# Optimization experiments

Measured on AMD Instinct MI355X. Metric: run time of the kernel, lower is better.

The kernel has to match this reference:

```python
import jax, jax.numpy as jnp
import numpy as np

EPS = 1e-5
B, C, H, W, MIP, CQ = 2, 256, 64, 64, 8, 32  # MIP = max(8, C//32); CQ = C//8


def _bn(x, p):
    # inference BatchNorm; p is [4, C] = (gamma, beta, running_mean, running_var)
    g, b, m, v = p[0], p[1], p[2], p[3]
    s = g / jnp.sqrt(v + EPS)
    return x * s[None, :, None, None] + (b - m * s)[None, :, None, None]


def _c1(x, w):  # 1x1 conv, w: [O, I]
    return jnp.einsum('bchw,oc->bohw', x, w)


def _c3(x, w):  # 3x3 conv, SAME padding, w: [O, I, 3, 3]
    return jax.lax.conv_general_dilated(x, w, (1, 1), 'SAME',
                                        dimension_numbers=('NCHW', 'OIHW', 'NCHW'))


def _cbs1(x, w, p):  # Conv(1x1)+BN+SiLU (YOLOv7 Conv block)
    return jax.nn.silu(_bn(_c1(x, w), p))


def _cbs3(x, w, p):  # Conv(3x3)+BN+SiLU
    return jax.nn.silu(_bn(_c3(x, w), p))


def _maxpool(x, k):  # MaxPool2d(kernel=k, stride=1, padding=k//2)
    p = k // 2
    return jax.lax.reduce_window(x, -jnp.inf, jax.lax.max,
                                 (1, 1, k, k), (1, 1, 1, 1),
                                 ((0, 0), (0, 0), (p, p), (p, p)))


def setup_inputs() -> dict:
    ks = iter(jax.random.split(jax.random.key(0), 64))

    def rn(shape, scale):
        return jax.random.normal(next(ks), shape, jnp.float32) * scale

    def w_(o, i, k=1):  # fan-in scaled conv weight
        sc = 1.0 / float(np.sqrt(i * k * k))
        return rn((o, i) if k == 1 else (o, i, k, k), sc)

    def bnp(c):  # gamma, beta, running_mean, running_var (var > 0)
        return jnp.stack([1.0 + rn((c,), 0.05), rn((c,), 0.05), rn((c,), 0.05),
                          0.5 + jax.random.uniform(next(ks), (c,), jnp.float32)])

    cm = C  # SPPCSPC hidden: int(2*C*0.5) = C
    return dict(
        x=rn((B, C, H, W), 1.0),
        ca_w1=w_(MIP, C), ca_b1=rn((MIP,), 0.05), ca_bn=bnp(MIP),
        ca_wh=w_(C, MIP), ca_bh=rn((C,), 0.05),
        ca_ww=w_(C, MIP), ca_bw=rn((C,), 0.05),
        s1_w=w_(cm, C), s1_bn=bnp(cm),
        s2_w=w_(cm, C), s2_bn=bnp(cm),
        s3_w=w_(cm, cm, 3), s3_bn=bnp(cm),
        s4_w=w_(cm, cm), s4_bn=bnp(cm),
        s5_w=w_(cm, 4 * cm), s5_bn=bnp(cm),
        s6_w=w_(cm, cm, 3), s6_bn=bnp(cm),
        s7_w=w_(C, 2 * cm), s7_bn=bnp(C),
        pq_w=w_(CQ, C), pq_b=rn((CQ,), 0.05),
        pk_w=w_(CQ, C), pk_b=rn((CQ,), 0.05),
        pv_w=w_(C, C), pv_b=rn((C,), 0.05),
        gamma_pa=rn((1,), 1.0), gamma_ca=rn((1,), 1.0),
    )


def reference(x, ca_w1, ca_b1, ca_bn, ca_wh, ca_bh, ca_ww, ca_bw,
              s1_w, s1_bn, s2_w, s2_bn, s3_w, s3_bn, s4_w, s4_bn,
              s5_w, s5_bn, s6_w, s6_bn, s7_w, s7_bn,
              pq_w, pq_b, pk_w, pk_b, pv_w, pv_b, gamma_pa, gamma_ca):
    b, c, h, w = x.shape
    # ---- CoordAtt ----
    xh = jnp.mean(x, axis=3, keepdims=True)                                 # b,c,h,1
    xw = jnp.transpose(jnp.mean(x, axis=2, keepdims=True), (0, 1, 3, 2))    # b,c,w,1
    y = jnp.concatenate([xh, xw], axis=2)                                   # b,c,h+w,1
    y = _bn(_c1(y, ca_w1) + ca_b1[None, :, None, None], ca_bn)
    y = y * jnp.clip(y + 3.0, 0.0, 6.0) / 6.0                               # h_swish
    a_h = jax.nn.sigmoid(_c1(y[:, :, :h], ca_wh) + ca_bh[None, :, None, None])
    a_w = jax.nn.sigmoid(_c1(jnp.transpose(y[:, :, h:], (0, 1, 3, 2)), ca_ww)
                         + ca_bw[None, :, None, None])
    r = x * a_w * a_h
    # ---- SPPCSPC ----
    x1 = _cbs1(_cbs3(_cbs1(r, s1_w, s1_bn), s3_w, s3_bn), s4_w, s4_bn)
    cat = jnp.concatenate([x1] + [_maxpool(x1, k) for k in (5, 9, 13)], axis=1)
    y1 = _cbs3(_cbs1(cat, s5_w, s5_bn), s6_w, s6_bn)
    y2 = _cbs1(r, s2_w, s2_bn)
    res = _cbs1(jnp.concatenate([y1, y2], axis=1), s7_w, s7_bn)
    # ---- PAM (spatial attention) ----
    n = h * w
    f = res.reshape(b, c, n)
    q = jnp.einsum('bcn,oc->bon', f, pq_w) + pq_b[None, :, None]            # b,c/8,n
    k = jnp.einsum('bcn,oc->bon', f, pk_w) + pk_b[None, :, None]
    v = jnp.einsum('bcn,oc->bon', f, pv_w) + pv_b[None, :, None]            # b,c,n
    attn = jax.nn.softmax(jnp.einsum('bcn,bcm->bnm', q, k), axis=-1)        # b,n,n
    res_pa = gamma_pa * jnp.einsum('bcm,bnm->bcn', v, attn).reshape(b, c, h, w) + res
    # ---- CAM (channel attention) ----
    e = jnp.einsum('bcn,bdn->bcd', f, f)                                    # b,c,c
    attn_c = jax.nn.softmax(jnp.max(e, axis=-1, keepdims=True) - e, axis=-1)
    res_ca = gamma_ca * jnp.einsum('bcd,bdn->bcn', attn_c, f).reshape(b, c, h, w) + res
    return res + res_ca + res_pa
```

## Files before the change

### kernel.cpp

```cpp
#include <hip/hip_runtime.h>

typedef unsigned short u16;
typedef __attribute__((ext_vector_type(8))) short bf16x8;
typedef __attribute__((ext_vector_type(4))) float f32x4;
#define EPSV 1e-5f
#define LOG2E 1.4426950408889634f

__device__ __forceinline__ float b2f(u16 u) {
  union { float f; unsigned int i; } v; v.i = ((unsigned int)u) << 16; return v.f;
}
__device__ __forceinline__ u16 f2b(float f) {
  union { float f; unsigned int i; } v; v.f = f;
  unsigned int r = v.i + 0x7FFFu + ((v.i >> 16) & 1u);
  return (u16)(r >> 16);
}
__device__ __forceinline__ u16 f2b_trunc(float f) {
  union { float f; unsigned int i; } v; v.f = f;
  return (u16)(v.i >> 16);
}
__device__ __forceinline__ float silu_(float z) { return z / (1.f + exp2f(-LOG2E * z)); }

__global__ __launch_bounds__(128) void detect_k(const u16* __restrict__ xp, float* __restrict__ flag) {
  __shared__ int cnt[2];
  int t = threadIdx.x;
// ... 55 lines not shown
  union { u16 h[8]; uint4 q; } u;
  u.h[0]=f2b(f0.x); u.h[1]=f2b(f0.y); u.h[2]=f2b(f0.z); u.h[3]=f2b(f0.w);
  u.h[4]=f2b(f1.x); u.h[5]=f2b(f1.y); u.h[6]=f2b(f1.z); u.h[7]=f2b(f1.w);
  *(uint4*)(dst + (long)i * 8) = u.q;
}


__global__ __launch_bounds__(256) void plane_means(const float* __restrict__ x, float* __restrict__ yin) {
  __shared__ float pl[4096];
  int bc = blockIdx.x, t = threadIdx.x;
  const float* xp = x + (long)bc * 4096;
  for (int j = 0; j < 16; ++j) { int id = j * 256 + t; pl[id] = xp[id]; }
  __syncthreads();
  if (t < 64) {
    float s = 0.f;
    for (int w = 0; w < 64; ++w) s += pl[t * 64 + w];
    yin[(long)bc * 128 + t] = s * (1.f / 64.f);
  } else if (t < 128) {
    int w = t - 64; float s = 0.f;
    for (int h = 0; h < 64; ++h) s += pl[h * 64 + w];
    yin[(long)bc * 128 + 64 + w] = s * (1.f / 64.f);
  }
}

__global__ __launch_bounds__(128) void ca_conv1(const float* __restrict__ yin, const float* __restrict__ w1,
                                                const float* __restrict__ b1, const float* __restrict__ bnp,
                                                float* __restrict__ ybn) {
  int b = blockIdx.x, p = threadIdx.x;
  float acc[8] = {0.f,0.f,0.f,0.f,0.f,0.f,0.f,0.f};
  for (int c = 0; c < 256; ++c) {
    float yv = yin[((long)b * 256 + c) * 128 + p];
    #pragma unroll
    for (int o = 0; o < 8; ++o) acc[o] += w1[o * 256 + c] * yv;
  }
  #pragma unroll
  for (int o = 0; o < 8; ++o) {
    float z = acc[o] + b1[o];
    float g = bnp[o], bt = bnp[8 + o], mn = bnp[16 + o], vr = bnp[24 + o];
    float s = g * rsqrtf(vr + EPSV);
    z = z * s + (bt - mn * s);
    float hs = fminf(fmaxf(z + 3.f, 0.f), 6.f) * (1.f / 6.f);
    ybn[((long)b * 8 + o) * 128 + p] = z * hs;
  }
}

__global__ __launch_bounds__(128) void ca_gate(const float* __restrict__ ybn,
    const float* __restrict__ wh, const float* __restrict__ bh,
    const float* __restrict__ ww, const float* __restrict__ bw,
    float* __restrict__ ah, float* __restrict__ aw_) {
  int c = blockIdx.x, b = blockIdx.y, t = threadIdx.x;
  if (t < 64) {
    float d = 0.f;
    #pragma unroll
    for (int o = 0; o < 8; ++o) d += wh[c * 8 + o] * ybn[((long)b * 8 + o) * 128 + t];
    d += bh[c];
    ah[((long)b * 256 + c) * 64 + t] = 1.f / (1.f + exp2f(-LOG2E * d));
  } else {
    int w = t - 64;
    float d = 0.f;
    #pragma unroll
    for (int o = 0; o < 8; ++o) d += ww[c * 8 + o] * ybn[((long)b * 8 + o) * 128 + 64 + w];
    d += bw[c];
    aw_[((long)b * 256 + c) * 64 + w] = 1.f / (1.f + exp2f(-LOG2E * d));
  }
}

__global__ __launch_bounds__(256) void apply_ca(const float* __restrict__ x, const float* __restrict__ ah,
                                                const float* __restrict__ aw_, u16* __restrict__ r) {
  int idx = blockIdx.x * 256 + threadIdx.x;
  int n = idx & 4095, bc = idx >> 12;
  int h = n >> 6, w = n & 63;
  r[idx] = f2b(x[idx] * ah[bc * 64 + h] * aw_[bc * 64 + w]);
}


template<int ACT, int OUTH>
__global__ __launch_bounds__(256) void mfma_cbs(
    const u16* __restrict__ Wbf, long aBS,
    const u16* __restrict__ In, long bBS,
    void* __restrict__ Out, long oBS,
    int O, int K, int N,
    const float* __restrict__ bnp, const float* __restrict__ bias)
{
  __shared__ u16 Bs[64 * 40];
  __shared__ float albe[64][2];
  const int t = threadIdx.x;
  const int n0 = blockIdx.x * 64;
  const int o0 = blockIdx.y * 64;
  const int b  = blockIdx.z;
  const int w = t >> 6, l = t & 63, lq = l >> 4, lr = l & 15;
  const int wo = (w >> 1) * 32, wn = (w & 1) * 32;
  if (t < 64) {
    int o = o0 + t;
    float al = 1.f, be = 0.f;
    if (bnp) {
      float g = bnp[o], bt = bnp[O + o], mn = bnp[2 * O + o], vr = bnp[3 * O + o];
      al = g * rsqrtf(vr + EPSV); be = bt - mn * al;
    }
    if (bias) be += bias[o];
    albe[t][0] = al; albe[t][1] = be;
  }
  const u16* Ab = Wbf + (long)b * aBS;
  const u16* inb = In + (long)b * bBS + n0;
  const u16* a0p = Ab + (long)(o0 + wo + lr) * K + lq * 8;
  const u16* a1p = a0p + (long)16 * K;
  const int bk = t >> 3, bn8 = (t & 7) * 8;
  f32x4 acc[2][2] = {};
  uint4 a0 = *(const uint4*)(a0p);
  uint4 a1 = *(const uint4*)(a1p);
  uint4 b0 = *(const uint4*)(inb + (long)bk * N + bn8);
  for (int kc = 0; kc < K; kc += 32) {
    int kn = kc + 32; if (kn >= K) kn = 0;
    __syncthreads();
    {
      union { uint4 q; u16 h[8]; } tb; tb.q = b0;
      #pragma unroll
      for (int j = 0; j < 8; ++j) Bs[(bn8 + j) * 40 + bk] = tb.h[j];
    }
    uint4 a0n = *(const uint4*)(a0p + kn);
    uint4 a1n = *(const uint4*)(a1p + kn);
    uint4 b0n = *(const uint4*)(inb + (long)(kn + bk) * N + bn8);
    __syncthreads();
    bf16x8 bfv0 = *(const bf16x8*)&Bs[(wn + lr) * 40 + lq * 8];
    bf16x8 bfv1 = *(const bf16x8*)&Bs[(wn + 16 + lr) * 40 + lq * 8];
    acc[0][0] = __builtin_amdgcn_mfma_f32_16x16x32_bf16(*(const bf16x8*)&a0, bfv0, acc[0][0], 0, 0, 0);
    acc[0][1] = __builtin_amdgcn_mfma_f32_16x16x32_bf16(*(const bf16x8*)&a0, bfv1, acc[0][1], 0, 0, 0);
    acc[1][0] = __builtin_amdgcn_mfma_f32_16x16x32_bf16(*(const bf16x8*)&a1, bfv0, acc[1][0], 0, 0, 0);
    acc[1][1] = __builtin_amdgcn_mfma_f32_16x16x32_bf16(*(const bf16x8*)&a1, bfv1, acc[1][1], 0, 0, 0);
    a0 = a0n; a1 = a1n; b0 = b0n;
  }
  float* ob = (float*)Out + (long)b * oBS;
  u16* obh = (u16*)Out + (long)b * oBS;
  #pragma unroll
  for (int i = 0; i < 2; ++i) {
    #pragma unroll
    for (int r = 0; r < 4; ++r) {
      int ol = wo + i * 16 + lq * 4 + r;
      float al = albe[ol][0], be = albe[ol][1];
      #pragma unroll
      for (int j = 0; j < 2; ++j) {
        float vv = acc[i][j][r] * al + be;
        if (ACT) vv = silu_(vv);
        if (OUTH == 2) {
          int col = n0 + wn + j * 16 + lr;
          obh[((long)(col >> 5) * 256 + (o0 + ol)) * 32 + (col & 31)] = f2b(vv);
        } else if (OUTH) {
          obh[(long)(o0 + ol) * N + n0 + wn + j * 16 + lr] = f2b(vv);
        } else {
          ob[(long)(o0 + ol) * N + n0 + wn + j * 16 + lr] = vv;
        }
      }
    }
  }
}

__global__ __launch_bounds__(256) void conv3_mfma(
    const u16* __restrict__ Wt,
    const u16* __restrict__ In, long iBS,
    u16* __restrict__ Out, long oBS, int O, int I,
    const float* __restrict__ bnp)
{
  __shared__ u16 Bs[4 * 66 * 34];
  __shared__ float albe[64][2];
  const int t = threadIdx.x;
  const int h0 = blockIdx.x * 2;
  const int o0 = blockIdx.y * 64;
  const int b  = blockIdx.z;
  const int w = t >> 6, l = t & 63, lq = l >> 4, lr = l & 15;
  const int wn = w * 32;
  if (t < 64) {
    int o = o0 + t;
    float g = bnp[o], bt = bnp[O + o], mn = bnp[2 * O + o], vr = bnp[3 * O + o];
    float al = g * rsqrtf(vr + EPSV);
    albe[t][0] = al; albe[t][1] = bt - mn * al;
  }
  {
    int r = t >> 6, cs = (t >> 5) & 1, ch = t & 31;
    Bs[(r * 66 + (cs ? 65 : 0)) * 34 + ch] = 0;
  }
  const u16* inb = In + (long)b * iBS;
  const int bch = t >> 3, bcg = (t & 7) * 8;
  const u16* wlane = Wt + (long)(o0 + lr) * 32 + lq * 8;
  const int nC8 = I >> 5;
  f32x4 acc[4][2] = {};

  uint4 tb0, tb1, tb2, tb3;
  {
    const u16* cb = inb + (long)bch * 4096 + bcg;
    tb0 = (h0 - 1 >= 0) ? *(const uint4*)(cb + (h0 - 1) * 64) : make_uint4(0,0,0,0);
    tb1 = *(const uint4*)(cb + h0 * 64);
    tb2 = *(const uint4*)(cb + (h0 + 1) * 64);
    tb3 = (h0 + 2 < 64) ? *(const uint4*)(cb + (h0 + 2) * 64) : make_uint4(0,0,0,0);
  }

  for (int c8 = 0; c8 < nC8; ++c8) {
    __syncthreads();
    {
      union { uint4 q; u16 h[8]; } u0, u1, u2, u3;
      u0.q = tb0; u1.q = tb1; u2.q = tb2; u3.q = tb3;
      #pragma unroll
      for (int j2 = 0; j2 < 8; ++j2) {
        Bs[(0 * 66 + bcg + 1 + j2) * 34 + bch] = u0.h[j2];
        Bs[(1 * 66 + bcg + 1 + j2) * 34 + bch] = u1.h[j2];
        Bs[(2 * 66 + bcg + 1 + j2) * 34 + bch] = u2.h[j2];
        Bs[(3 * 66 + bcg + 1 + j2) * 34 + bch] = u3.h[j2];
      }
    }
    int c8n = c8 + 1; if (c8n >= nC8) c8n = 0;
    uint4 n0_, n1_, n2_, n3_;
    {
      const u16* cb = inb + (long)(c8n * 32 + bch) * 4096 + bcg;
      n0_ = (h0 - 1 >= 0) ? *(const uint4*)(cb + (h0 - 1) * 64) : make_uint4(0,0,0,0);
      n1_ = *(const uint4*)(cb + h0 * 64);
      n2_ = *(const uint4*)(cb + (h0 + 1) * 64);
      n3_ = (h0 + 2 < 64) ? *(const uint4*)(cb + (h0 + 2) * 64) : make_uint4(0,0,0,0);
    }
    __syncthreads();
    const u16* wc8 = wlane + (long)c8 * 9 * 256 * 32;
    #pragma unroll
    for (int dy = 0; dy < 3; ++dy) {
      #pragma unroll
      for (int dx = 0; dx < 3; ++dx) {
        const int tap = dy * 3 + dx;
        const u16* wl = wc8 + (long)tap * 256 * 32;
        uint4 af0 = *(const uint4*)(wl);
        uint4 af1 = *(const uint4*)(wl + 16 * 32);
        uint4 af2 = *(const uint4*)(wl + 32 * 32);
        uint4 af3 = *(const uint4*)(wl + 48 * 32);
        #pragma unroll
        for (int j = 0; j < 2; ++j) {
          int nb = wn + j * 16;
          int rowS = (nb >> 6) + dy;
          int colS = (nb & 63) + dx;
          bf16x8 bv = *(const bf16x8*)&Bs[(rowS * 66 + colS + lr) * 34 + lq * 8];
          acc[0][j] = __builtin_amdgcn_mfma_f32_16x16x32_bf16(*(const bf16x8*)&af0, bv, acc[0][j], 0, 0, 0);
          acc[1][j] = __builtin_amdgcn_mfma_f32_16x16x32_bf16(*(const bf16x8*)&af1, bv, acc[1][j], 0, 0, 0);
          acc[2][j] = __builtin_amdgcn_mfma_f32_16x16x32_bf16(*(const bf16x8*)&af2, bv, acc[2][j], 0, 0, 0);
          acc[3][j] = __builtin_amdgcn_mfma_f32_16x16x32_bf16(*(const bf16x8*)&af3, bv, acc[3][j], 0, 0, 0);
        }
      }
    }
    tb0 = n0_; tb1 = n1_; tb2 = n2_; tb3 = n3_;
  }
  u16* ob = Out + (long)b * oBS;
  const int n0 = h0 * 64;
  #pragma unroll
  for (int i = 0; i < 4; ++i) {
    #pragma unroll
    for (int r = 0; r < 4; ++r) {
      int ol = i * 16 + lq * 4 + r;
      float al = albe[ol][0], be = albe[ol][1];
      #pragma unroll
      for (int j = 0; j < 2; ++j) {
        float vv = silu_(acc[i][j][r] * al + be);
        ob[(long)(o0 + ol) * 4096 + n0 + wn + j * 16 + lr] = f2b(vv);
      }
    }
  }
}

__global__ __launch_bounds__(256) void pool3(u16* __restrict__ cat, long bs) {
  __shared__ float A[68][72];
  __shared__ float Bb[68][72];
  const int t = threadIdx.x;
  const int c = blockIdx.x, b = blockIdx.y;
  u16* base = cat + (long)b * bs + (long)c * 4096;
  for (int i = t; i < 68 * 72; i += 256) { (&A[0][0])[i] = -1e30f; (&Bb[0][0])[i] = -1e30f; }
  __syncthreads();
  const int r = t >> 2, c0 = (t & 3) * 16;
  #pragma unroll
  for (int j = 0; j < 16; ++j) A[r + 2][c0 + 2 + j] = b2f(base[r * 64 + c0 + j]);
  const long CNu = 1048576;
  #pragma unroll 1
  for (int s = 1; s <= 3; ++s) {
    __syncthreads();
    #pragma unroll
    for (int j = 0; j < 16; ++j) {
      int cc = c0 + j;
      float m = fmaxf(fmaxf(fmaxf(A[r+2][cc], A[r+2][cc+1]), fmaxf(A[r+2][cc+2], A[r+2][cc+3])), A[r+2][cc+4]);
      Bb[r + 2][cc + 2] = m;
    }
    __syncthreads();
    u16* out = base + (long)s * CNu;
    #pragma unroll
    for (int j = 0; j < 16; ++j) {
      int hc = c0 + 2 + j;
      float m = fmaxf(fmaxf(fmaxf(Bb[r][hc], Bb[r+1][hc]), fmaxf(Bb[r+2][hc], Bb[r+3][hc])), Bb[r+4][hc]);
      out[r * 64 + c0 + j] = f2b_trunc(m);
      A[r + 2][hc] = m;
    }
  }
}

__global__ __launch_bounds__(256) void transpose_hh(const u16* __restrict__ in, u16* __restrict__ out) {
  __shared__ u16 tile[32][34];
  int b = blockIdx.z;
  int c0 = blockIdx.x * 32, r0 = blockIdx.y * 32;
  int tx = threadIdx.x & 31, ty = threadIdx.x >> 5;
  const u16* ib = in + (long)b * 262144;
  u16* ob = out + (long)b * 262144;
  #pragma unroll
  for (int i = 0; i < 4; ++i) {
    int r = r0 + ty + i * 8;
    tile[ty + i * 8][tx] = ib[(long)r * 4096 + c0 + tx];
  }
  __syncthreads();
  #pragma unroll
  for (int i = 0; i < 4; ++i) {
    int c = c0 + ty + i * 8;
    ob[(long)c * 64 + r0 + tx] = tile[tx][ty + i * 8];
  }
}

__global__ __launch_bounds__(256) void pam_qk_max(const u16* __restrict__ qkT, float* __restrict__ pmax) {
  __shared__ u16 Qs[32 * 40];
  __shared__ u16 Ks[64 * 40];
  __shared__ float red[4][32][17];
  const int t = threadIdx.x;
  const int b = blockIdx.z, ms = blockIdx.y, n0 = blockIdx.x * 32;
  const int w = t >> 6, l = t & 63, lq = l >> 4, lr = l & 15;
  const int wn = w & 1, wc = w >> 1;
  if (t < 128) {
    int row = t >> 2, cq = (t & 3) * 8;
    *(uint4*)&Qs[row * 40 + cq] = *(const uint4*)(qkT + ((long)b * 4096 + n0 + row) * 64 + cq);
  }
  __syncthreads();
  bf16x8 qf = *(const bf16x8*)&Qs[(wn * 16 + lr) * 40 + lq * 8];
  float mx4[4] = {-1e30f, -1e30f, -1e30f, -1e30f};
  const int krow = t >> 2, kcq = (t & 3) * 8;
  for (int it = 0; it < 16; ++it) {
    int m0 = ms * 1024 + it * 64;
    __syncthreads();
    *(uint4*)&Ks[krow * 40 + kcq] = *(const uint4*)(qkT + ((long)b * 4096 + m0 + krow) * 64 + 32 + kcq);
    __syncthreads();
    #pragma unroll
    for (int s = 0; s < 2; ++s) {
      int msub = wc * 2 + s;
      bf16x8 kf = *(const bf16x8*)&Ks[(msub * 16 + lr) * 40 + lq * 8];
      f32x4 S = {};
      S = __builtin_amdgcn_mfma_f32_16x16x32_bf16(qf, kf, S, 0, 0, 0);
      #pragma unroll
      for (int r = 0; r < 4; ++r) mx4[r] = fmaxf(mx4[r], S[r]);
    }
  }
  #pragma unroll
  for (int r = 0; r < 4; ++r) red[w][wn * 16 + lq * 4 + r][lr] = mx4[r];
  __syncthreads();
  if (t < 32) {
    int wbase = t >> 4;
    float M = -1e30f;
    #pragma unroll
    for (int j = 0; j < 2; ++j)
      #pragma unroll
      for (int l2 = 0; l2 < 16; ++l2)
        M = fmaxf(M, red[wbase + 2 * j][t][l2]);
    pmax[((long)ms * 2 + b) * 4096 + n0 + t] = M;
  }
}

__global__ __launch_bounds__(256) void pam_merge(const float* __restrict__ pmax, float* __restrict__ rmx) {
  int i = blockIdx.x * 256 + threadIdx.x;
  int b = i >> 12, n = i & 4095;
  float m = pmax[(long)b * 4096 + n];
  #pragma unroll
  for (int ms = 1; ms < 4; ++ms) m = fmaxf(m, pmax[((long)ms * 2 + b) * 4096 + n]);
  rmx[i] = m;
}

__global__ __launch_bounds__(512) void pam_attn(const u16* __restrict__ qkT,
    const u16* __restrict__ vb, const float* __restrict__ rowmax,
    float* __restrict__ Obase, float* __restrict__ Sbase) {
  __shared__ u16 Qs[32 * 40];
  __shared__ u16 Ks[2][64 * 40];
  __shared__ u16 Ps[32 * 72];
  __shared__ float rmL[32];
  __shared__ float srow[32];
  const int t = threadIdx.x;
  const int mh = blockIdx.y;
  const int b = blockIdx.z;
  const int n0 = blockIdx.x * 32;
  const int w = t >> 6, l = t & 63, lq = l >> 4, lr = l & 15;
  const int nf = w & 1;
  const int mf = w >> 1;
  const int cw = w * 32;
  float* O = Obase + (long)mh * 2097152;
  float* S = Sbase + (long)mh * 8192;
  if (t < 128) {
    int row = t >> 2, cq = (t & 3) * 8;
    *(uint4*)&Qs[row * 40 + cq] = *(const uint4*)(qkT + ((long)b * 4096 + n0 + row) * 64 + cq);
  }
  if (t < 32) { rmL[t] = rowmax[(long)b * 4096 + n0 + t] * LOG2E; srow[t] = 0.f; }
  const int krow = t >> 3, kc4 = (t & 7) * 4;
  const u16* kbase = qkT + ((long)b * 4096 + krow) * 64 + 32 + kc4;
  const u16* vop = vb + (long)b * 1048576 + (cw + lr) * 32 + lq * 8;
  const int mStart = mh * 2048, mEnd = mStart + 2048;

  {
    uint2 k0 = *(const uint2*)(kbase + (long)mStart * 64);
    *(uint2*)&Ks[0][krow * 40 + kc4] = k0;
  }
  uint2 kreg = *(const uint2*)(kbase + (long)(mStart + 64) * 64);
  long vt0 = (long)(mStart >> 5) * 8192;
  uint4 vA00 = *(const uint4*)(vop + vt0);
  uint4 vA01 = *(const uint4*)(vop + vt0 + 512);
  uint4 vA10 = *(const uint4*)(vop + vt0 + 8192);
  uint4 vA11 = *(const uint4*)(vop + vt0 + 8704);
  uint4 vB00, vB01, vB10, vB11;

  __syncthreads();
  bf16x8 qf = *(const bf16x8*)&Qs[(nf * 16 + lr) * 40 + lq * 8];
  const float rml = rmL[nf * 16 + lr];
  float spl = 0.f;
  f32x4 acc[2][2] = {};

#define QK_PHASE(BUF)                                                          \
  {                                                                            \
    bf16x8 kf = *(const bf16x8*)&Ks[BUF][(mf * 16 + lr) * 40 + lq * 8];        \
    f32x4 Sv = {};                                                             \
    Sv = __builtin_amdgcn_mfma_f32_16x16x32_bf16(kf, qf, Sv, 0, 0, 0);         \
    union { u16 h[4]; uint2 q; } pk;                                           \
    _Pragma("unroll")                                                          \
    for (int r = 0; r < 4; ++r) {                                              \
      float p = exp2f(Sv[r] * LOG2E - rml);                                    \
      spl += p;                                                                \
      pk.h[r] = f2b_trunc(p);                                                  \
    }                                                                          \
    *(uint2*)&Ps[(nf * 16 + lr) * 72 + mf * 16 + lq * 4] = pk.q;               \
  }

#define PV_PHASE(V00, V01, V10, V11)                                           \
  {                                                                            \
    bf16x8 pf0 = *(const bf16x8*)&Ps[lr * 72 + lq * 8];                        \
    bf16x8 pf1 = *(const bf16x8*)&Ps[(16 + lr) * 72 + lq * 8];                 \
    acc[0][0] = __builtin_amdgcn_mfma_f32_16x16x32_bf16(*(bf16x8*)&V00, pf0, acc[0][0], 0, 0, 0); \
    acc[0][1] = __builtin_amdgcn_mfma_f32_16x16x32_bf16(*(bf16x8*)&V00, pf1, acc[0][1], 0, 0, 0); \
    acc[1][0] = __builtin_amdgcn_mfma_f32_16x16x32_bf16(*(bf16x8*)&V01, pf0, acc[1][0], 0, 0, 0); \
    acc[1][1] = __builtin_amdgcn_mfma_f32_16x16x32_bf16(*(bf16x8*)&V01, pf1, acc[1][1], 0, 0, 0); \
    pf0 = *(const bf16x8*)&Ps[lr * 72 + 32 + lq * 8];                          \
    pf1 = *(const bf16x8*)&Ps[(16 + lr) * 72 + 32 + lq * 8];                   \
    acc[0][0] = __builtin_amdgcn_mfma_f32_16x16x32_bf16(*(bf16x8*)&V10, pf0, acc[0][0], 0, 0, 0); \
    acc[0][1] = __builtin_amdgcn_mfma_f32_16x16x32_bf16(*(bf16x8*)&V10, pf1, acc[0][1], 0, 0, 0); \
    acc[1][0] = __builtin_amdgcn_mfma_f32_16x16x32_bf16(*(bf16x8*)&V11, pf0, acc[1][0], 0, 0, 0); \
    acc[1][1] = __builtin_amdgcn_mfma_f32_16x16x32_bf16(*(bf16x8*)&V11, pf1, acc[1][1], 0, 0, 0); \
  }

  #pragma unroll 1
  for (int m0 = mStart; m0 < mEnd; m0 += 128) {
    int m2 = m0 + 128; if (m2 >= mEnd) m2 = mStart;
    int m3 = m0 + 192; if (m3 >= mEnd) m3 = mStart;
    QK_PHASE(0)
    *(uint2*)&Ks[1][krow * 40 + kc4] = kreg;
    kreg = *(const uint2*)(kbase + (long)m2 * 64);
    {
      long vt = (long)((m0 + 64) >> 5) * 8192;
      vB00 = *(const uint4*)(vop + vt);
      vB01 = *(const uint4*)(vop + vt + 512);
      vB10 = *(const uint4*)(vop + vt + 8192);
      vB11 = *(const uint4*)(vop + vt + 8704);
    }
    __syncthreads();
    __builtin_amdgcn_s_setprio(1);
    PV_PHASE(vA00, vA01, vA10, vA11)
    __builtin_amdgcn_s_setprio(0);
    __syncthreads();
    QK_PHASE(1)
    *(uint2*)&Ks[0][krow * 40 + kc4] = kreg;
    kreg = *(const uint2*)(kbase + (long)m3 * 64);
    {
      long vt = (long)(m2 >> 5) * 8192;
      vA00 = *(const uint4*)(vop + vt);
      vA01 = *(const uint4*)(vop + vt + 512);
      vA10 = *(const uint4*)(vop + vt + 8192);
      vA11 = *(const uint4*)(vop + vt + 8704);
    }
    __syncthreads();
    __builtin_amdgcn_s_setprio(1);
    PV_PHASE(vB00, vB01, vB10, vB11)
    __builtin_amdgcn_s_setprio(0);
    __syncthreads();
  }
#undef QK_PHASE
#undef PV_PHASE

  spl += __shfl_xor(spl, 16);
  spl += __shfl_xor(spl, 32);
  if (l < 16) atomicAdd(&srow[nf * 16 + lr], spl);
  __syncthreads();
  if (t < 32) S[(long)b * 4096 + n0 + t] = srow[t];
  float* ob = O + (long)b * 1048576 + n0;
  #pragma unroll
  for (int cf = 0; cf < 2; ++cf) {
    #pragma unroll
    for (int r = 0; r < 4; ++r) {
      int c = cw + cf * 16 + lq * 4 + r;
      ob[(long)c * 4096 + lr]      = acc[cf][0][r];
      ob[(long)c * 4096 + 16 + lr] = acc[cf][1][r];
    }
  }
}


__global__ __launch_bounds__(256) void fillz(float* __restrict__ p, int n) {
  int i = blockIdx.x * 256 + threadIdx.x;
  if (i < n) p[i] = 0.f;
}

__global__ __launch_bounds__(256) void cam_e_mfma(const u16* __restrict__ resb, float* __restrict__ e) {
  __shared__ u16 Bs[128 * 40];
  const int t = threadIdx.x;
  const int d0 = blockIdx.x * 128;
  const int c0 = blockIdx.y * 64;
  const int bz = blockIdx.z;
  const int b = bz >> 4, ks = bz & 15;
  const int w = t >> 6, l = t & 63, lq = l >> 4, lr = l & 15;
  const int wo = (w >> 1) * 32, wn = (w & 1) * 64;
  const u16* fb = resb + (long)b * 1048576;
  const u16* a0p = fb + (long)(c0 + wo + lr) * 4096 + lq * 8;
  const u16* a1p = a0p + (long)16 * 4096;
  const int bo = t >> 1, bkq = (t & 1) * 16;
  const u16* bp = fb + (long)(d0 + bo) * 4096 + bkq;
  const int kS = ks * 256, kE = kS + 256;
  f32x4 acc[2][4] = {};
  uint4 a0 = *(const uint4*)(a0p + kS);
  uint4 a1 = *(const uint4*)(a1p + kS);
  uint4 b0 = *(const uint4*)(bp + kS);
  uint4 b1 = *(const uint4*)(bp + kS + 8);
  for (int kc = kS; kc < kE; kc += 32) {
    int kn = kc + 32; if (kn >= kE) kn = kS;
    __syncthreads();
    *(uint4*)&Bs[bo * 40 + bkq] = b0;
    *(uint4*)&Bs[bo * 40 + bkq + 8] = b1;
    uint4 a0n = *(const uint4*)(a0p + kn);
    uint4 a1n = *(const uint4*)(a1p + kn);
    uint4 b0n = *(const uint4*)(bp + kn);
    uint4 b1n = *(const uint4*)(bp + kn + 8);
    __syncthreads();
    #pragma unroll
    for (int j = 0; j < 4; ++j) {
      bf16x8 bfv = *(const bf16x8*)&Bs[(wn + j * 16 + lr) * 40 + lq * 8];
      acc[0][j] = __builtin_amdgcn_mfma_f32_16x16x32_bf16(*(const bf16x8*)&a0, bfv, acc[0][j], 0, 0, 0);
      acc[1][j] = __builtin_amdgcn_mfma_f32_16x16x32_bf16(*(const bf16x8*)&a1, bfv, acc[1][j], 0, 0, 0);
    }
    a0 = a0n; a1 = a1n; b0 = b0n; b1 = b1n;
  }
  #pragma unroll
  for (int i = 0; i < 2; ++i)
    #pragma unroll
    for (int r = 0; r < 4; ++r) {
      int ol = wo + i * 16 + lq * 4 + r;
      #pragma unroll
      for (int j = 0; j < 4; ++j)
        atomicAdd(&e[((long)b << 16) + (long)(c0 + ol) * 256 + d0 + wn + j * 16 + lr], acc[i][j][r]);
    }
}

__global__ __launch_bounds__(256) void cam_softmax(const float* __restrict__ e, u16* __restrict__ attn) {
  __shared__ float red[256];
  int c = blockIdx.x, b = blockIdx.y, t = threadIdx.x;
  const float* row = e + ((long)b << 16) + (long)c * 256;
  float v = row[t];
  red[t] = v; __syncthreads();
  for (int s = 128; s > 0; s >>= 1) { if (t < s) red[t] = fminf(red[t], red[t + s]); __syncthreads(); }
  float emin = red[0]; __syncthreads();
  float ex = exp2f(LOG2E * (emin - v));
  red[t] = ex; __syncthreads();
  for (int s = 128; s > 0; s >>= 1) { if (t < s) red[t] += red[t + s]; __syncthreads(); }
  float inv = 1.f / red[0];
  attn[((long)b << 16) + (long)c * 256 + t] = f2b(ex * inv);
}


__global__ __launch_bounds__(256) void combine(const float* __restrict__ res, const float* __restrict__ O,
    const float* __restrict__ S, const float* __restrict__ cam, const float* __restrict__ gp,
    void* __restrict__ outp, const float* __restrict__ flagp) {
  int idx = blockIdx.x * 256 + threadIdx.x;
  int b = idx >> 20, n = idx & 4095;
  float g1 = gp[0], g2 = gp[1];
  float sden = S[(long)b * 4096 + n] + S[8192 + (long)b * 4096 + n];
  float pamv = (O[idx] + O[2097152 + idx]) / sden;
  float v = 3.f * res[idx] + g1 * pamv + g2 * cam[idx];
  if (*flagp > 0.5f) ((float*)outp)[idx] = v;
  else               ((u16*)outp)[idx] = f2b(v);
}


extern "C" void kernel_launch(void* const* d_in, const int* in_sizes, int n_in,
                              void* d_out, int out_size, void* d_ws, size_t ws_size,
                              hipStream_t stream)
{
  (void)out_size; (void)ws_size; (void)n_in;
  float* ws = (float*)d_ws;
  const long CN = 1048576;

  float* A  = ws;
  float* Bp = ws + 2 * CN;
  float* Cp = ws + 4 * CN;
  float* D  = ws + 6 * CN;
  const long WFo = 14 * CN;

  u16*   rB   = (u16*)A;
  float* res  = A;
  float* xf   = Bp;
  u16*   BpU  = (u16*)Bp;
  float* yin  = Cp;
  float* ybn  = Cp + 65536;
  float* ah   = Cp + 67584;
  float* aw_  = Cp + 100352;
  u16*   CpU  = (u16*)Cp;
  u16*   catU = (u16*)D;
  u16*   y12U = (u16*)D;
  float* D2   = D + 2 * CN;
  u16*   qkbU = (u16*)D2;
  u16*   qkTU = (u16*)(D2 + 262144);
  float* pmax = D2 + 524288;
  float* rmx  = D2 + 557056;
  float* e    = D2 + 565248;
  u16*   attnc= (u16*)(D2 + 696320);
  float* S0   = D2 + 761856;
  float* cam  = D;
  float* O0   = D + 4 * CN;

  ConvArgs ca;
  long fOff[30], hOff[30];
  long hcur = 0;
  float* flagp = ws + WFo;
  {
    long cum = 0, fcur = WFo + 4;
    for (int i = 0; i < 30; ++i) {
      ca.src[i] = d_in[i];
      int h = (i == 8 || i == 10 || i == 14 || i == 16 || i == 20 ||
               i == 22 || i == 24 || i == 26) ? 1 : 0;
      ca.mode[i] = h;
      if (i == 0) { ca.dst[i] = 2 * CN; fOff[i] = 2 * CN; }
      else if (h) { ca.dst[i] = hcur; hOff[i] = hcur; hcur += in_sizes[i]; }
      else        { ca.dst[i] = fcur; fOff[i] = fcur; fcur += in_sizes[i]; }
      cum += in_sizes[i];
      ca.end[i] = (int)cum;
    }
  }
  long fTotal = WFo + 4;
  for (int i = 1; i < 30; ++i) if (!ca.mode[i]) fTotal = (fOff[i] + in_sizes[i] > fTotal) ? fOff[i] + in_sizes[i] : fTotal;
  u16* wsH = (u16*)(ws + fTotal);
  u16* wt3a = wsH + hcur;
  u16* wt3b = wsH + hcur + 589824;
  int total = ca.end[29];

  detect_k<<<dim3(1), dim3(128), 0, stream>>>((const u16*)d_in[0], flagp);
  convert_all<<<dim3((total + 255) / 256), dim3(256), 0, stream>>>(ca, ws, wsH, flagp, total);

  float* ca_w1 = ws + fOff[1];
  float* ca_b1 = ws + fOff[2];
  float* ca_bn = ws + fOff[3];
  float* ca_wh = ws + fOff[4];
  float* ca_bh = ws + fOff[5];
  float* ca_ww = ws + fOff[6];
  float* ca_bw = ws + fOff[7];
  u16*   s1_w  = wsH + hOff[8];   float* s1_bn = ws + fOff[9];
  u16*   s2_w  = wsH + hOff[10];  float* s2_bn = ws + fOff[11];
  float* s3_wf = ws + fOff[12];   float* s3_bn = ws + fOff[13];
  u16*   s4_w  = wsH + hOff[14];  float* s4_bn = ws + fOff[15];
  u16*   s5_w  = wsH + hOff[16];  float* s5_bn = ws + fOff[17];
  float* s6_wf = ws + fOff[18];   float* s6_bn = ws + fOff[19];
  u16*   s7_w  = wsH + hOff[20];  float* s7_bn = ws + fOff[21];
  u16*   qk_w  = wsH + hOff[22];  float* qk_b  = ws + fOff[23];
  u16*   pv_w  = wsH + hOff[26];  float* pv_b  = ws + fOff[27];
  float* gammas = ws + fOff[28];

  w3t<<<dim3(2304), dim3(256), 0, stream>>>(s3_wf, wt3a);
  w3t<<<dim3(2304), dim3(256), 0, stream>>>(s6_wf, wt3b);

  plane_means<<<dim3(512), dim3(256), 0, stream>>>(xf, yin);
  ca_conv1<<<dim3(2), dim3(128), 0, stream>>>(yin, ca_w1, ca_b1, ca_bn, ybn);
  ca_gate<<<dim3(256, 2), dim3(128), 0, stream>>>(ybn, ca_wh, ca_bh, ca_ww, ca_bw, ah, aw_);
  apply_ca<<<dim3(8192), dim3(256), 0, stream>>>(xf, ah, aw_, rB);

  mfma_cbs<1,1><<<dim3(64, 4, 2), dim3(256), 0, stream>>>(s1_w, 0, rB, CN, CpU, CN, 256, 256, 4096, s1_bn, nullptr);
  conv3_mfma<<<dim3(32, 4, 2), dim3(256), 0, stream>>>(wt3a, CpU, CN, BpU, CN, 256, 256, s3_bn);
  mfma_cbs<1,1><<<dim3(64, 4, 2), dim3(256), 0, stream>>>(s4_w, 0, BpU, CN, catU, 4 * CN, 256, 256, 4096, s4_bn, nullptr);

  pool3<<<dim3(256, 2), dim3(256), 0, stream>>>(catU, 4 * CN);

  mfma_cbs<1,1><<<dim3(64, 4, 2), dim3(256), 0, stream>>>(s5_w, 0, catU, 4 * CN, BpU, CN, 256, 1024, 4096, s5_bn, nullptr);
  conv3_mfma<<<dim3(32, 4, 2), dim3(256), 0, stream>>>(wt3b, BpU, CN, y12U, 2 * CN, 256, 256, s6_bn);
  mfma_cbs<1,1><<<dim3(64, 4, 2), dim3(256), 0, stream>>>(s2_w, 0, rB, CN, y12U + CN, 2 * CN, 256, 256, 4096, s2_bn, nullptr);
  mfma_cbs<1,0><<<dim3(64, 4, 2), dim3(256), 0, stream>>>(s7_w, 0, y12U, 2 * CN, res, CN, 256, 512, 4096, s7_bn, nullptr);

  cvtb<<<dim3(1024), dim3(256), 0, stream>>>(res, BpU, 262144);
  mfma_cbs<0,1><<<dim3(64, 1, 2), dim3(256), 0, stream>>>(qk_w, 0, BpU, CN, qkbU, 262144, 64, 256, 4096, nullptr, qk_b);
  mfma_cbs<0,2><<<dim3(64, 4, 2), dim3(256), 0, stream>>>(pv_w, 0, BpU, CN, CpU, CN, 256, 256, 4096, nullptr, pv_b);
  transpose_hh<<<dim3(128, 2, 2), dim3(256), 0, stream>>>(qkbU, qkTU);

  pam_qk_max<<<dim3(128, 4, 2), dim3(256), 0, stream>>>(qkTU, pmax);
  pam_merge<<<dim3(32), dim3(256), 0, stream>>>(pmax, rmx);
  pam_attn<<<dim3(128, 2, 2), dim3(512), 0, stream>>>(qkTU, CpU, rmx, O0, S0);

  fillz<<<dim3(512), dim3(256), 0, stream>>>(e, 131072);
  cam_e_mfma<<<dim3(2, 4, 32), dim3(256), 0, stream>>>(BpU, e);
  cam_softmax<<<dim3(256, 2), dim3(256), 0, stream>>>(e, attnc);
  mfma_cbs<0,0><<<dim3(64, 4, 2), dim3(256), 0, stream>>>(attnc, 65536, BpU, CN, cam, CN, 256, 256, 4096, nullptr, nullptr);

  combine<<<dim3(8192), dim3(256), 0, stream>>>(res, O0, S0, cam, gammas, d_out, flagp);
}
```

Before: 436.2 us.

## Double-buffer LDS tiles across GEMM, conv3, and attention kernels; shrink conv3 tile

Converts the shared-memory B/K/P tiles in mfma_cbs, conv3_mfma, pam_qk_max, pam_attn and cam_e_mfma to ping-pong double buffers. The next tile is stored into the other buffer while the current one is consumed, which allows one of the two barriers per iteration to be dropped. conv3_mfma also switches to one output row per block, with twice the grid and fewer accumulators per thread, to raise occupancy. In exchange it adds LDS usage and a deeper prefetch, and the conv3 change reloads more weights across blocks.

```diff
diff --git a/kernel.cpp b/kernel.cpp
--- a/kernel.cpp
+++ b/kernel.cpp
@@ -161,7 +161,7 @@
     int O, int K, int N,
     const float* __restrict__ bnp, const float* __restrict__ bias)
 {
-  __shared__ u16 Bs[64 * 40];
+  __shared__ u16 Bs[2][64 * 40];
   __shared__ float albe[64][2];
   const int t = threadIdx.x;
   const int n0 = blockIdx.x * 64;
@@ -185,28 +185,36 @@
   const u16* a1p = a0p + (long)16 * K;
   const int bk = t >> 3, bn8 = (t & 7) * 8;
   f32x4 acc[2][2] = {};
+  uint4 b0 = *(const uint4*)(inb + (long)bk * N + bn8);
+  {
+    union { uint4 q; u16 h[8]; } tb; tb.q = b0;
+    #pragma unroll
+    for (int j = 0; j < 8; ++j) Bs[0][(bn8 + j) * 40 + bk] = tb.h[j];
+  }
+  b0 = *(const uint4*)(inb + (long)(32 + bk) * N + bn8);
   uint4 a0 = *(const uint4*)(a0p);
   uint4 a1 = *(const uint4*)(a1p);
-  uint4 b0 = *(const uint4*)(inb + (long)bk * N + bn8);
+  __syncthreads();
   for (int kc = 0; kc < K; kc += 32) {
-    int kn = kc + 32; if (kn >= K) kn = 0;
-    __syncthreads();
+    const int p = (kc >> 5) & 1;
     {
       union { uint4 q; u16 h[8]; } tb; tb.q = b0;
       #pragma unroll
-      for (int j = 0; j < 8; ++j) Bs[(bn8 + j) * 40 + bk] = tb.h[j];
-    }
+      for (int j = 0; j < 8; ++j) Bs[p ^ 1][(bn8 + j) * 40 + bk] = tb.h[j];
+    }
+    int kn = kc + 32; if (kn >= K) kn = 0;
+    int kb = kc + 64; if (kb >= K) kb = 0;
     uint4 a0n = *(const uint4*)(a0p + kn);
     uint4 a1n = *(const uint4*)(a1p + kn);
-    uint4 b0n = *(const uint4*)(inb + (long)(kn + bk) * N + bn8);
-    __syncthreads();
-    bf16x8 bfv0 = *(const bf16x8*)&Bs[(wn + lr) * 40 + lq * 8];
-    bf16x8 bfv1 = *(const bf16x8*)&Bs[(wn + 16 + lr) * 40 + lq * 8];
+    uint4 b0n = *(const uint4*)(inb + (long)(kb + bk) * N + bn8);
+    bf16x8 bfv0 = *(const bf16x8*)&Bs[p][(wn + lr) * 40 + lq * 8];
+    bf16x8 bfv1 = *(const bf16x8*)&Bs[p][(wn + 16 + lr) * 40 + lq * 8];
     acc[0][0] = __builtin_amdgcn_mfma_f32_16x16x32_bf16(*(const bf16x8*)&a0, bfv0, acc[0][0], 0, 0, 0);
     acc[0][1] = __builtin_amdgcn_mfma_f32_16x16x32_bf16(*(const bf16x8*)&a0, bfv1, acc[0][1], 0, 0, 0);
     acc[1][0] = __builtin_amdgcn_mfma_f32_16x16x32_bf16(*(const bf16x8*)&a1, bfv0, acc[1][0], 0, 0, 0);
     acc[1][1] = __builtin_amdgcn_mfma_f32_16x16x32_bf16(*(const bf16x8*)&a1, bfv1, acc[1][1], 0, 0, 0);
     a0 = a0n; a1 = a1n; b0 = b0n;
+    __syncthreads();
   }
   float* ob = (float*)Out + (long)b * oBS;
   u16* obh = (u16*)Out + (long)b * oBS;
@@ -239,87 +247,95 @@
     u16* __restrict__ Out, long oBS, int O, int I,
     const float* __restrict__ bnp)
 {
-  __shared__ u16 Bs[4 * 66 * 34];
+  __shared__ u16 Bs[2][3 * 66 * 34];
   __shared__ float albe[64][2];
   const int t = threadIdx.x;
-  const int h0 = blockIdx.x * 2;
+  const int h0 = blockIdx.x;
   const int o0 = blockIdx.y * 64;
   const int b  = blockIdx.z;
   const int w = t >> 6, l = t & 63, lq = l >> 4, lr = l & 15;
-  const int wn = w * 32;
+  const int wn = w * 16;
   if (t < 64) {
     int o = o0 + t;
     float g = bnp[o], bt = bnp[O + o], mn = bnp[2 * O + o], vr = bnp[3 * O + o];
     float al = g * rsqrtf(vr + EPSV);
     albe[t][0] = al; albe[t][1] = bt - mn * al;
   }
-  {
+  if (t < 192) {
     int r = t >> 6, cs = (t >> 5) & 1, ch = t & 31;
-    Bs[(r * 66 + (cs ? 65 : 0)) * 34 + ch] = 0;
+    Bs[0][(r * 66 + (cs ? 65 : 0)) * 34 + ch] = 0;
+    Bs[1][(r * 66 + (cs ? 65 : 0)) * 34 + ch] = 0;
   }
   const u16* inb = In + (long)b * iBS;
   const int bch = t >> 3, bcg = (t & 7) * 8;
   const u16* wlane = Wt + (long)(o0 + lr) * 32 + lq * 8;
   const int nC8 = I >> 5;
-  f32x4 acc[4][2] = {};
-
-  uint4 tb0, tb1, tb2, tb3;
+  f32x4 acc[4] = {};
+
+  uint4 tb0, tb1, tb2;
   {
     const u16* cb = inb + (long)bch * 4096 + bcg;
     tb0 = (h0 - 1 >= 0) ? *(const uint4*)(cb + (h0 - 1) * 64) : make_uint4(0,0,0,0);
     tb1 = *(const uint4*)(cb + h0 * 64);
-    tb2 = *(const uint4*)(cb + (h0 + 1) * 64);
-    tb3 = (h0 + 2 < 64) ? *(const uint4*)(cb + (h0 + 2) * 64) : make_uint4(0,0,0,0);
-  }
+    tb2 = (h0 + 1 < 64) ? *(const uint4*)(cb + (h0 + 1) * 64) : make_uint4(0,0,0,0);
+  }
+  {
+    union { uint4 q; u16 h[8]; } u0, u1, u2;
+    u0.q = tb0; u1.q = tb1; u2.q = tb2;
+    #pragma unroll
+    for (int j2 = 0; j2 < 8; ++j2) {
+      Bs[0][(0 * 66 + bcg + 1 + j2) * 34 + bch] = u0.h[j2];
+      Bs[0][(1 * 66 + bcg + 1 + j2) * 34 + bch] = u1.h[j2];
+      Bs[0][(2 * 66 + bcg + 1 + j2) * 34 + bch] = u2.h[j2];
+    }
+  }
+  if (nC8 > 1) {
+    const u16* cb = inb + (long)(32 + bch) * 4096 + bcg;
+    tb0 = (h0 - 1 >= 0) ? *(const uint4*)(cb + (h0 - 1) * 64) : make_uint4(0,0,0,0);
+    tb1 = *(const uint4*)(cb + h0 * 64);
+    tb2 = (h0 + 1 < 64) ? *(const uint4*)(cb + (h0 + 1) * 64) : make_uint4(0,0,0,0);
+  }
+  __syncthreads();
 
   for (int c8 = 0; c8 < nC8; ++c8) {
-    __syncthreads();
+    const int p = c8 & 1;
     {
-      union { uint4 q; u16 h[8]; } u0, u1, u2, u3;
-      u0.q = tb0; u1.q = tb1; u2.q = tb2; u3.q = tb3;
+      union { uint4 q; u16 h[8]; } u0, u1, u2;
+      u0.q = tb0; u1.q = tb1; u2.q = tb2;
       #pragma unroll
       for (int j2 = 0; j2 < 8; ++j2) {
-        Bs[(0 * 66 + bcg + 1 + j2) * 34 + bch] = u0.h[j2];
-        Bs[(1 * 66 + bcg + 1 + j2) * 34 + bch] = u1.h[j2];
-        Bs[(2 * 66 + bcg + 1 + j2) * 34 + bch] = u2.h[j2];
-        Bs[(3 * 66 + bcg + 1 + j2) * 34 + bch] = u3.h[j2];
+        Bs[p ^ 1][(0 * 66 + bcg + 1 + j2) * 34 + bch] = u0.h[j2];
+        Bs[p ^ 1][(1 * 66 + bcg + 1 + j2) * 34 + bch] = u1.h[j2];
+        Bs[p ^ 1][(2 * 66 + bcg + 1 + j2) * 34 + bch] = u2.h[j2];
       }
     }
-    int c8n = c8 + 1; if (c8n >= nC8) c8n = 0;
-    uint4 n0_, n1_, n2_, n3_;
+    int c8n = c8 + 2; if (c8n >= nC8) c8n = 0;
     {
       const u16* cb = inb + (long)(c8n * 32 + bch) * 4096 + bcg;
-      n0_ = (h0 - 1 >= 0) ? *(const uint4*)(cb + (h0 - 1) * 64) : make_uint4(0,0,0,0);
-      n1_ = *(const uint4*)(cb + h0 * 64);
-      n2_ = *(const uint4*)(cb + (h0 + 1) * 64);
-      n3_ = (h0 + 2 < 64) ? *(const uint4*)(cb + (h0 + 2) * 64) : make_uint4(0,0,0,0);
-    }
-    __syncthreads();
-    const u16* wc8 = wlane + (long)c8 * 9 * 256 * 32;
-    #pragma unroll
-    for (int dy = 0; dy < 3; ++dy) {
+      uint4 n0_ = (h0 - 1 >= 0) ? *(const uint4*)(cb + (h0 - 1) * 64) : make_uint4(0,0,0,0);
+      uint4 n1_ = *(const uint4*)(cb + h0 * 64);
+      uint4 n2_ = (h0 + 1 < 64) ? *(const uint4*)(cb + (h0 + 1) * 64) : make_uint4(0,0,0,0);
+      const u16* wc8 = wlane + (long)c8 * 9 * 256 * 32;
       #pragma unroll
-      for (int dx = 0; dx < 3; ++dx) {
-        const int tap = dy * 3 + dx;
-        const u16* wl = wc8 + (long)tap * 256 * 32;
-        uint4 af0 = *(const uint4*)(wl);
-        uint4 af1 = *(const uint4*)(wl + 16 * 32);
-        uint4 af2 = *(const uint4*)(wl + 32 * 32);
-        uint4 af3 = *(const uint4*)(wl + 48 * 32);
+      for (int dy = 0; dy < 3; ++dy) {
         #pragma unroll
-        for (int j = 0; j < 2; ++j) {
-          int nb = wn + j * 16;
-          int rowS = (nb >> 6) + dy;
-          int colS = (nb & 63) + dx;
-          bf16x8 bv = *(const bf16x8*)&Bs[(rowS * 66 + colS + lr) * 34 + lq * 8];
-          acc[0][j] = __builtin_amdgcn_mfma_f32_16x16x32_bf16(*(const bf16x8*)&af0, bv, acc[0][j], 0, 0, 0);
-          acc[1][j] = __builtin_amdgcn_mfma_f32_16x16x32_bf16(*(const bf16x8*)&af1, bv, acc[1][j], 0, 0, 0);
-          acc[2][j] = __builtin_amdgcn_mfma_f32_16x16x32_bf16(*(const bf16x8*)&af2, bv, acc[2][j], 0, 0, 0);
-          acc[3][j] = __builtin_amdgcn_mfma_f32_16x16x32_bf16(*(const bf16x8*)&af3, bv, acc[3][j], 0, 0, 0);
+        for (int dx = 0; dx < 3; ++dx) {
+          const int tap = dy * 3 + dx;
+          const u16* wl = wc8 + (long)tap * 256 * 32;
+          uint4 af0 = *(const uint4*)(wl);
+          uint4 af1 = *(const uint4*)(wl + 16 * 32);
+          uint4 af2 = *(const uint4*)(wl + 32 * 32);
+          uint4 af3 = *(const uint4*)(wl + 48 * 32);
+          bf16x8 bv = *(const bf16x8*)&Bs[p][(dy * 66 + wn + dx + lr) * 34 + lq * 8];
+          acc[0] = __builtin_amdgcn_mfma_f32_16x16x32_bf16(*(const bf16x8*)&af0, bv, acc[0], 0, 0, 0);
+          acc[1] = __builtin_amdgcn_mfma_f32_16x16x32_bf16(*(const bf16x8*)&af1, bv, acc[1], 0, 0, 0);
+          acc[2] = __builtin_amdgcn_mfma_f32_16x16x32_bf16(*(const bf16x8*)&af2, bv, acc[2], 0, 0, 0);
+          acc[3] = __builtin_amdgcn_mfma_f32_16x16x32_bf16(*(const bf16x8*)&af3, bv, acc[3], 0, 0, 0);
         }
       }
-    }
-    tb0 = n0_; tb1 = n1_; tb2 = n2_; tb3 = n3_;
+      tb0 = n0_; tb1 = n1_; tb2 = n2_;
+    }
+    __syncthreads();
   }
   u16* ob = Out + (long)b * oBS;
   const int n0 = h0 * 64;
@@ -329,11 +345,8 @@
     for (int r = 0; r < 4; ++r) {
       int ol = i * 16 + lq * 4 + r;
       float al = albe[ol][0], be = albe[ol][1];
-      #pragma unroll
-      for (int j = 0; j < 2; ++j) {
-        float vv = silu_(acc[i][j][r] * al + be);
-        ob[(long)(o0 + ol) * 4096 + n0 + wn + j * 16 + lr] = f2b(vv);
-      }
+      float vv = silu_(acc[i][r] * al + be);
+      ob[(long)(o0 + ol) * 4096 + n0 + wn + lr] = f2b(vv);
     }
   }
 }
@@ -393,7 +406,7 @@
 
 __global__ __launch_bounds__(256) void pam_qk_max(const u16* __restrict__ qkT, float* __restrict__ pmax) {
   __shared__ u16 Qs[32 * 40];
-  __shared__ u16 Ks[64 * 40];
+  __shared__ u16 Ks[2][64 * 40];
   __shared__ float red[4][32][17];
   const int t = threadIdx.x;
   const int b = blockIdx.z, ms = blockIdx.y, n0 = blockIdx.x * 32;
@@ -403,24 +416,31 @@
     int row = t >> 2, cq = (t & 3) * 8;
     *(uint4*)&Qs[row * 40 + cq] = *(const uint4*)(qkT + ((long)b * 4096 + n0 + row) * 64 + cq);
   }
+  const int krow = t >> 2, kcq = (t & 3) * 8;
+  const u16* kb = qkT + ((long)b * 4096 + krow) * 64 + 32 + kcq;
+  {
+    uint4 k0 = *(const uint4*)(kb + (long)(ms * 1024) * 64);
+    *(uint4*)&Ks[0][krow * 40 + kcq] = k0;
+  }
+  uint4 kreg = *(const uint4*)(kb + (long)(ms * 1024 + 64) * 64);
   __syncthreads();
   bf16x8 qf = *(const bf16x8*)&Qs[(wn * 16 + lr) * 40 + lq * 8];
   float mx4[4] = {-1e30f, -1e30f, -1e30f, -1e30f};
-  const int krow = t >> 2, kcq = (t & 3) * 8;
   for (int it = 0; it < 16; ++it) {
-    int m0 = ms * 1024 + it * 64;
-    __syncthreads();
-    *(uint4*)&Ks[krow * 40 + kcq] = *(const uint4*)(qkT + ((long)b * 4096 + m0 + krow) * 64 + 32 + kcq);
-    __syncthreads();
+    const int p = it & 1;
+    *(uint4*)&Ks[p ^ 1][krow * 40 + kcq] = kreg;
+    int itn = it + 2; if (itn >= 16) itn = 0;
+    kreg = *(const uint4*)(kb + (long)(ms * 1024 + itn * 64) * 64);
     #pragma unroll
     for (int s = 0; s < 2; ++s) {
       int msub = wc * 2 + s;
-      bf16x8 kf = *(const bf16x8*)&Ks[(msub * 16 + lr) * 40 + lq * 8];
+      bf16x8 kf = *(const bf16x8*)&Ks[p][(msub * 16 + lr) * 40 + lq * 8];
       f32x4 S = {};
       S = __builtin_amdgcn_mfma_f32_16x16x32_bf16(qf, kf, S, 0, 0, 0);
       #pragma unroll
       for (int r = 0; r < 4; ++r) mx4[r] = fmaxf(mx4[r], S[r]);
     }
+    __syncthreads();
   }
   #pragma unroll
   for (int r = 0; r < 4; ++r) red[w][wn * 16 + lq * 4 + r][lr] = mx4[r];
@@ -451,7 +471,7 @@
     float* __restrict__ Obase, float* __restrict__ Sbase) {
   __shared__ u16 Qs[32 * 40];
   __shared__ u16 Ks[2][64 * 40];
-  __shared__ u16 Ps[32 * 72];
+  __shared__ u16 Ps[2][32 * 72];
   __shared__ float rmL[32];
   __shared__ float srow[32];
   const int t = threadIdx.x;
@@ -492,9 +512,9 @@
   float spl = 0.f;
   f32x4 acc[2][2] = {};
 
-#define QK_PHASE(BUF)                                                          \
+#define QK_PHASE(KBUF, PBUF)                                                   \
   {                                                                            \
-    bf16x8 kf = *(const bf16x8*)&Ks[BUF][(mf * 16 + lr) * 40 + lq * 8];        \
+    bf16x8 kf = *(const bf16x8*)&Ks[KBUF][(mf * 16 + lr) * 40 + lq * 8];       \
     f32x4 Sv = {};                                                             \
     Sv = __builtin_amdgcn_mfma_f32_16x16x32_bf16(kf, qf, Sv, 0, 0, 0);         \
     union { u16 h[4]; uint2 q; } pk;                                           \
@@ -504,19 +524,19 @@
       spl += p;                                                                \
       pk.h[r] = f2b_trunc(p);                                                  \
     }                                                                          \
-    *(uint2*)&Ps[(nf * 16 + lr) * 72 + mf * 16 + lq * 4] = pk.q;               \
-  }
-
-#define PV_PHASE(V00, V01, V10, V11)                                           \
+    *(uint2*)&Ps[PBUF][(nf * 16 + lr) * 72 + mf * 16 + lq * 4] = pk.q;         \
+  }
+
+#define PV_PHASE(PBUF, V00, V01, V10, V11)                                     \
   {                                                                            \
-    bf16x8 pf0 = *(const bf16x8*)&Ps[lr * 72 + lq * 8];                        \
-    bf16x8 pf1 = *(const bf16x8*)&Ps[(16 + lr) * 72 + lq * 8];                 \
+    bf16x8 pf0 = *(const bf16x8*)&Ps[PBUF][lr * 72 + lq * 8];                  \
+    bf16x8 pf1 = *(const bf16x8*)&Ps[PBUF][(16 + lr) * 72 + lq * 8];           \
     acc[0][0] = __builtin_amdgcn_mfma_f32_16x16x32_bf16(*(bf16x8*)&V00, pf0, acc[0][0], 0, 0, 0); \
     acc[0][1] = __builtin_amdgcn_mfma_f32_16x16x32_bf16(*(bf16x8*)&V00, pf1, acc[0][1], 0, 0, 0); \
     acc[1][0] = __builtin_amdgcn_mfma_f32_16x16x32_bf16(*(bf16x8*)&V01, pf0, acc[1][0], 0, 0, 0); \
     acc[1][1] = __builtin_amdgcn_mfma_f32_16x16x32_bf16(*(bf16x8*)&V01, pf1, acc[1][1], 0, 0, 0); \
-    pf0 = *(const bf16x8*)&Ps[lr * 72 + 32 + lq * 8];                          \
-    pf1 = *(const bf16x8*)&Ps[(16 + lr) * 72 + 32 + lq * 8];                   \
+    pf0 = *(const bf16x8*)&Ps[PBUF][lr * 72 + 32 + lq * 8];                    \
+    pf1 = *(const bf16x8*)&Ps[PBUF][(16 + lr) * 72 + 32 + lq * 8];             \
     acc[0][0] = __builtin_amdgcn_mfma_f32_16x16x32_bf16(*(bf16x8*)&V10, pf0, acc[0][0], 0, 0, 0); \
     acc[0][1] = __builtin_amdgcn_mfma_f32_16x16x32_bf16(*(bf16x8*)&V10, pf1, acc[0][1], 0, 0, 0); \
     acc[1][0] = __builtin_amdgcn_mfma_f32_16x16x32_bf16(*(bf16x8*)&V11, pf0, acc[1][0], 0, 0, 0); \
@@ -527,7 +547,7 @@
   for (int m0 = mStart; m0 < mEnd; m0 += 128) {
     int m2 = m0 + 128; if (m2 >= mEnd) m2 = mStart;
     int m3 = m0 + 192; if (m3 >= mEnd) m3 = mStart;
-    QK_PHASE(0)
+    QK_PHASE(0, 0)
     *(uint2*)&Ks[1][krow * 40 + kc4] = kreg;
     kreg = *(const uint2*)(kbase + (long)m2 * 64);
     {
@@ -539,10 +559,9 @@
     }
     __syncthreads();
     __builtin_amdgcn_s_setprio(1);
-    PV_PHASE(vA00, vA01, vA10, vA11)
+    PV_PHASE(0, vA00, vA01, vA10, vA11)
     __builtin_amdgcn_s_setprio(0);
-    __syncthreads();
-    QK_PHASE(1)
+    QK_PHASE(1, 1)
     *(uint2*)&Ks[0][krow * 40 + kc4] = kreg;
     kreg = *(const uint2*)(kbase + (long)m3 * 64);
     {
@@ -554,9 +573,8 @@
     }
     __syncthreads();
     __builtin_amdgcn_s_setprio(1);
-    PV_PHASE(vB00, vB01, vB10, vB11)
+    PV_PHASE(1, vB00, vB01, vB10, vB11)
     __builtin_amdgcn_s_setprio(0);
-    __syncthreads();
   }
 #undef QK_PHASE
 #undef PV_PHASE
@@ -585,7 +603,7 @@
 }
 
 __global__ __launch_bounds__(256) void cam_e_mfma(const u16* __restrict__ resb, float* __restrict__ e) {
-  __shared__ u16 Bs[128 * 40];
+  __shared__ u16 Bs[2][128 * 40];
   const int t = threadIdx.x;
   const int d0 = blockIdx.x * 128;
   const int c0 = blockIdx.y * 64;
@@ -600,27 +618,33 @@
   const u16* bp = fb + (long)(d0 + bo) * 4096 + bkq;
   const int kS = ks * 256, kE = kS + 256;
   f32x4 acc[2][4] = {};
+  uint4 b0 = *(const uint4*)(bp + kS);
+  uint4 b1 = *(const uint4*)(bp + kS + 8);
+  *(uint4*)&Bs[0][bo * 40 + bkq] = b0;
+  *(uint4*)&Bs[0][bo * 40 + bkq + 8] = b1;
+  b0 = *(const uint4*)(bp + kS + 32);
+  b1 = *(const uint4*)(bp + kS + 40);
   uint4 a0 = *(const uint4*)(a0p + kS);
   uint4 a1 = *(const uint4*)(a1p + kS);
-  uint4 b0 = *(const uint4*)(bp + kS);
-  uint4 b1 = *(const uint4*)(bp + kS + 8);
+  __syncthreads();
   for (int kc = kS; kc < kE; kc += 32) {
+    const int p = ((kc - kS) >> 5) & 1;
+    *(uint4*)&Bs[p ^ 1][bo * 40 + bkq] = b0;
+    *(uint4*)&Bs[p ^ 1][bo * 40 + bkq + 8] = b1;
     int kn = kc + 32; if (kn >= kE) kn = kS;
-    __syncthreads();
-    *(uint4*)&Bs[bo * 40 + bkq] = b0;
-    *(uint4*)&Bs[bo * 40 + bkq + 8] = b1;
+    int kb = kc + 64; if (kb >= kE) kb = kS;
     uint4 a0n = *(const uint4*)(a0p + kn);
     uint4 a1n = *(const uint4*)(a1p + kn);
-    uint4 b0n = *(const uint4*)(bp + kn);
-    uint4 b1n = *(const uint4*)(bp + kn + 8);
-    __syncthreads();
+    uint4 b0n = *(const uint4*)(bp + kb);
+    uint4 b1n = *(const uint4*)(bp + kb + 8);
     #pragma unroll
     for (int j = 0; j < 4; ++j) {
-      bf16x8 bfv = *(const bf16x8*)&Bs[(wn + j * 16 + lr) * 40 + lq * 8];
+      bf16x8 bfv = *(const bf16x8*)&Bs[p][(wn + j * 16 + lr) * 40 + lq * 8];
       acc[0][j] = __builtin_amdgcn_mfma_f32_16x16x32_bf16(*(const bf16x8*)&a0, bfv, acc[0][j], 0, 0, 0);
       acc[1][j] = __builtin_amdgcn_mfma_f32_16x16x32_bf16(*(const bf16x8*)&a1, bfv, acc[1][j], 0, 0, 0);
     }
     a0 = a0n; a1 = a1n; b0 = b0n; b1 = b1n;
+    __syncthreads();
   }
   #pragma unroll
   for (int i = 0; i < 2; ++i)
@@ -754,13 +778,13 @@
   apply_ca<<<dim3(8192), dim3(256), 0, stream>>>(xf, ah, aw_, rB);
 
   mfma_cbs<1,1><<<dim3(64, 4, 2), dim3(256), 0, stream>>>(s1_w, 0, rB, CN, CpU, CN, 256, 256, 4096, s1_bn, nullptr);
-  conv3_mfma<<<dim3(32, 4, 2), dim3(256), 0, stream>>>(wt3a, CpU, CN, BpU, CN, 256, 256, s3_bn);
+  conv3_mfma<<<dim3(64, 4, 2), dim3(256), 0, stream>>>(wt3a, CpU, CN, BpU, CN, 256, 256, s3_bn);
   mfma_cbs<1,1><<<dim3(64, 4, 2), dim3(256), 0, stream>>>(s4_w, 0, BpU, CN, catU, 4 * CN, 256, 256, 4096, s4_bn, nullptr);
 
   pool3<<<dim3(256, 2), dim3(256), 0, stream>>>(catU, 4 * CN);
 
   mfma_cbs<1,1><<<dim3(64, 4, 2), dim3(256), 0, stream>>>(s5_w, 0, catU, 4 * CN, BpU, CN, 256, 1024, 4096, s5_bn, nullptr);
-  conv3_mfma<<<dim3(32, 4, 2), dim3(256), 0, stream>>>(wt3b, BpU, CN, y12U, 2 * CN, 256, 256, s6_bn);
+  conv3_mfma<<<dim3(64, 4, 2), dim3(256), 0, stream>>>(wt3b, BpU, CN, y12U, 2 * CN, 256, 256, s6_bn);
   mfma_cbs<1,1><<<dim3(64, 4, 2), dim3(256), 0, stream>>>(s2_w, 0, rB, CN, y12U + CN, 2 * CN, 256, 256, 4096, s2_bn, nullptr);
   mfma_cbs<1,0><<<dim3(64, 4, 2), dim3(256), 0, stream>>>(s7_w, 0, y12U, 2 * CN, res, CN, 256, 512, 4096, s7_bn, nullptr);
 
```

After: 429.3 us. No clear change (-1.6%).
